# Performance work log

Measured on AMD Instinct MI355X. Metric: run time of the kernel, lower is better.

The kernel has to match this reference:

```python
import jax, jax.numpy as jnp
import numpy as np

B, L, T = 256, 1024, 128


def setup_inputs() -> dict:
    key = jax.random.key(0)
    k1, k2, k3, k4 = jax.random.split(key, 4)
    inputs = jax.random.normal(k1, (B, L, T), dtype=jnp.float32)
    lengths = jax.random.randint(k2, (B,), 1, L + 1, dtype=jnp.int32)
    tags = jax.random.randint(k3, (B, L), 0, T, dtype=jnp.int32)
    # learned CRF transition matrix (random_normal_initializer default stddev=0.05)
    transition_params = jax.random.normal(k4, (T, T), dtype=jnp.float32) * 0.05
    return {"inputs": inputs, "lengths": lengths, "tags": tags,
            "transition_params": transition_params}


def _crf_decode(x, trans, lengths):
    """Viterbi decode. x: [B,L,T], trans: [T,T], lengths: [B] -> tags [B,L] int32."""
    Bx, Lx, Tx = x.shape

    def fwd_step(state, inp):
        x_t, t = inp  # x_t: [B,T]
        scores = state[:, :, None] + trans[None]          # [B, T_prev, T_cur]
        bp = jnp.argmax(scores, axis=1).astype(jnp.int32)  # [B,T]
        new_state = jnp.max(scores, axis=1) + x_t           # [B,T]
        m = (t < lengths)[:, None]
        state = jnp.where(m, new_state, state)
        bp = jnp.where(m, bp, 0)
        return state, bp

    init = x[:, 0]                                          # [B,T]
    xs = (jnp.swapaxes(x[:, 1:], 0, 1), jnp.arange(1, Lx))
    state, bps = jax.lax.scan(fwd_step, init, xs)           # bps: [L-1,B,T]
    bps = jnp.concatenate([jnp.zeros((1, Bx, Tx), jnp.int32), bps], axis=0)  # bp[0] unused
    last_tag = jnp.argmax(state, axis=-1).astype(jnp.int32)  # [B] tag at position length-1

    def bwd_step(carry, inp):
        bp_t, t = inp
        emit = jnp.where(t < lengths, carry, 0)             # tags beyond length -> 0
        prev = jnp.take_along_axis(bp_t, carry[:, None], axis=1)[:, 0]
        carry = jnp.where((t > 0) & (t < lengths), prev, carry)
        return carry, emit

    _, tags_rev = jax.lax.scan(bwd_step, last_tag, (bps[::-1], jnp.arange(Lx)[::-1]))
    return jnp.swapaxes(tags_rev[::-1], 0, 1)               # [B,L]


def reference(inputs, lengths, tags, transition_params):
    # Decoder.call: tfa.text.crf_decode(inputs, transition_params, lengths)[0]
    return _crf_decode(inputs, transition_params, lengths)
```

## Files before the change

kernel.cpp:

```cpp
#include <hip/hip_runtime.h>

#define BB 256
#define LL 1024
#define TT 128
#define NTH 512

__device__ __forceinline__ void lds_barrier() {
    asm volatile("s_waitcnt lgkmcnt(0)\n\ts_barrier" ::);
}

struct SmallSmem {
    float state[TT];
    float pv[NTH];
    int   pi[NTH];
    unsigned char tags[LL];
};

__global__ __launch_bounds__(NTH)
void viterbi_kernel(const float* __restrict__ x,
                    const int* __restrict__ lengths,
                    const float* __restrict__ trans,
                    int* __restrict__ out) {
    __shared__ SmallSmem sm;
    extern __shared__ unsigned char bp[];

    const int b   = blockIdx.x;
    const int tid = threadIdx.x;
    const int j   = tid & (TT - 1);
    const int q   = tid >> 7;

    int lenb = lengths[b];
    if (lenb < 1) lenb = 1;
    if (lenb > LL) lenb = LL;

    float tc[32];
    #pragma unroll
    for (int ii = 0; ii < 32; ++ii)
        tc[ii] = trans[(q * 32 + ii) * TT + j];

    const float* xb = x + (size_t)b * LL * TT;

    if (tid < TT) sm.state[tid] = xb[tid];

    float xv_cur = 0.0f, xv_next = 0.0f;
    if (tid < TT && lenb > 1) xv_cur = xb[TT + j];
    lds_barrier();

    for (int t = 1; t < lenb; ++t) {
        if (tid < TT) {
            int tn = (t + 1 < lenb) ? (t + 1) : (lenb - 1);
            xv_next = xb[tn * TT + j];
        }

        float best0 = -3.4e38f, best1 = -3.4e38f, best2 = -3.4e38f, best3 = -3.4e38f;
        int   bi0 = 0, bi1 = 1, bi2 = 2, bi3 = 3;
        const float4* st4 = reinterpret_cast<const float4*>(sm.state + q * 32);
        #pragma unroll
        for (int k = 0; k < 8; ++k) {
            float4 sv = st4[k];
            float s0 = sv.x + tc[4 * k + 0];
            float s1 = sv.y + tc[4 * k + 1];
            float s2 = sv.z + tc[4 * k + 2];
            float s3 = sv.w + tc[4 * k + 3];
            if (s0 > best0) { best0 = s0; bi0 = 4 * k + 0; }
            if (s1 > best1) { best1 = s1; bi1 = 4 * k + 1; }
            if (s2 > best2) { best2 = s2; bi2 = 4 * k + 2; }
            if (s3 > best3) { best3 = s3; bi3 = 4 * k + 3; }
        }
        float bb = best0; int bi = bi0;
        if (best1 > bb || (best1 == bb && bi1 < bi)) { bb = best1; bi = bi1; }
        if (best2 > bb || (best2 == bb && bi2 < bi)) { bb = best2; bi = bi2; }
        if (best3 > bb || (best3 == bb && bi3 < bi)) { bb = best3; bi = bi3; }
        sm.pv[tid] = bb;
        sm.pi[tid] = bi + q * 32;
        lds_barrier();

        if (tid < TT) {
            float bv = sm.pv[j];       int ix = sm.pi[j];
            float v1 = sm.pv[j + 128]; int i1 = sm.pi[j + 128];
            float v2 = sm.pv[j + 256]; int i2 = sm.pi[j + 256];
            float v3 = sm.pv[j + 384]; int i3 = sm.pi[j + 384];
            if (v1 > bv) { bv = v1; ix = i1; }
            if (v2 > bv) { bv = v2; ix = i2; }
            if (v3 > bv) { bv = v3; ix = i3; }
            sm.state[j] = bv + xv_cur;
            bp[t * TT + j] = (unsigned char)ix;
            xv_cur = xv_next;
        }
        lds_barrier();
    }

    if (tid == 0) {
        float bv = sm.state[0]; int ix = 0;
        for (int i = 1; i < TT; ++i) {
            float v = sm.state[i];
            if (v > bv) { bv = v; ix = i; }
        }
        int carry = ix;
        for (int t = lenb - 1; t >= 1; --t) {
            sm.tags[t] = (unsigned char)carry;
            carry = bp[t * TT + carry];
        }
        sm.tags[0] = (unsigned char)carry;
    }
    lds_barrier();

    int* outb = out + (size_t)b * LL;
    for (int t = tid; t < LL; t += NTH)
        outb[t] = (t < lenb) ? (int)sm.tags[t] : 0;
}

extern "C" void kernel_launch(void* const* d_in, const int* in_sizes, int n_in,
                              void* d_out, int out_size, void* d_ws, size_t ws_size,
                              hipStream_t stream) {
    const float* x       = (const float*)d_in[0];
    const int*   lengths = (const int*)d_in[1];
    const float* trans   = (const float*)d_in[3];
    int*         out     = (int*)d_out;

    const int dyn = LL * TT;
    hipFuncSetAttribute((const void*)&viterbi_kernel,
                        hipFuncAttributeMaxDynamicSharedMemorySize, dyn);
    viterbi_kernel<<<BB, NTH, dyn, stream>>>(x, lengths, trans, out);
}
```

Measured before the change: 934.7 us.

## Double block threads and reduce argmax partials across lanes with shuffles

Raises the block size from 512 to 1024 threads, so each thread scans 16 predecessor states instead of 32. The second-stage reduction of the 8 partial maxima now runs across all threads, with each group of 8 lanes combining partials through xor shuffles. This replaces the serial 4-way combine done by only 128 threads. The partial arrays are padded (stride 132) to avoid LDS bank conflicts. The cost is more threads per barrier and a shuffle tree on every sequential timestep.

```diff
diff --git a/kernel.cpp b/kernel.cpp
--- a/kernel.cpp
+++ b/kernel.cpp
@@ -3,7 +3,10 @@
 #define BB 256
 #define LL 1024
 #define TT 128
-#define NTH 512
+#define NTH 1024
+#define NG 8
+#define PG 16
+#define PVS 132
 
 __device__ __forceinline__ void lds_barrier() {
     asm volatile("s_waitcnt lgkmcnt(0)\n\ts_barrier" ::);
@@ -11,8 +14,8 @@
 
 struct SmallSmem {
     float state[TT];
-    float pv[NTH];
-    int   pi[NTH];
+    float pv[NG * PVS];
+    int   pi[NG * PVS];
     unsigned char tags[LL];
 };
 
@@ -27,66 +30,69 @@
     const int b   = blockIdx.x;
     const int tid = threadIdx.x;
     const int j   = tid & (TT - 1);
-    const int q   = tid >> 7;
+    const int g   = tid >> 7;
+    const int jm  = tid >> 3;
+    const int wm  = tid & 7;
 
     int lenb = lengths[b];
     if (lenb < 1) lenb = 1;
     if (lenb > LL) lenb = LL;
 
-    float tc[32];
+    float tc[PG];
     #pragma unroll
-    for (int ii = 0; ii < 32; ++ii)
-        tc[ii] = trans[(q * 32 + ii) * TT + j];
+    for (int ii = 0; ii < PG; ++ii)
+        tc[ii] = trans[(g * PG + ii) * TT + j];
 
     const float* xb = x + (size_t)b * LL * TT;
 
     if (tid < TT) sm.state[tid] = xb[tid];
 
     float xv_cur = 0.0f, xv_next = 0.0f;
-    if (tid < TT && lenb > 1) xv_cur = xb[TT + j];
+    if (lenb > 1) xv_cur = xb[TT + jm];
     lds_barrier();
 
     for (int t = 1; t < lenb; ++t) {
-        if (tid < TT) {
+        {
             int tn = (t + 1 < lenb) ? (t + 1) : (lenb - 1);
-            xv_next = xb[tn * TT + j];
+            xv_next = xb[tn * TT + jm];
         }
 
-        float best0 = -3.4e38f, best1 = -3.4e38f, best2 = -3.4e38f, best3 = -3.4e38f;
-        int   bi0 = 0, bi1 = 1, bi2 = 2, bi3 = 3;
-        const float4* st4 = reinterpret_cast<const float4*>(sm.state + q * 32);
+        float a0 = -3.4e38f, a1 = -3.4e38f, a2 = -3.4e38f, a3 = -3.4e38f;
+        int   i0 = 0, i1 = 1, i2 = 2, i3 = 3;
+        const float4* st4 = reinterpret_cast<const float4*>(sm.state + g * PG);
         #pragma unroll
-        for (int k = 0; k < 8; ++k) {
+        for (int k = 0; k < 4; ++k) {
             float4 sv = st4[k];
             float s0 = sv.x + tc[4 * k + 0];
             float s1 = sv.y + tc[4 * k + 1];
             float s2 = sv.z + tc[4 * k + 2];
             float s3 = sv.w + tc[4 * k + 3];
-            if (s0 > best0) { best0 = s0; bi0 = 4 * k + 0; }
-            if (s1 > best1) { best1 = s1; bi1 = 4 * k + 1; }
-            if (s2 > best2) { best2 = s2; bi2 = 4 * k + 2; }
-            if (s3 > best3) { best3 = s3; bi3 = 4 * k + 3; }
+            if (s0 > a0) { a0 = s0; i0 = 4 * k + 0; }
+            if (s1 > a1) { a1 = s1; i1 = 4 * k + 1; }
+            if (s2 > a2) { a2 = s2; i2 = 4 * k + 2; }
+            if (s3 > a3) { a3 = s3; i3 = 4 * k + 3; }
         }
-        float bb = best0; int bi = bi0;
-        if (best1 > bb || (best1 == bb && bi1 < bi)) { bb = best1; bi = bi1; }
-        if (best2 > bb || (best2 == bb && bi2 < bi)) { bb = best2; bi = bi2; }
-        if (best3 > bb || (best3 == bb && bi3 < bi)) { bb = best3; bi = bi3; }
-        sm.pv[tid] = bb;
-        sm.pi[tid] = bi + q * 32;
+        float av = a0; int ax = i0;
+        if (a1 > av || (a1 == av && i1 < ax)) { av = a1; ax = i1; }
+        if (a2 > av || (a2 == av && i2 < ax)) { av = a2; ax = i2; }
+        if (a3 > av || (a3 == av && i3 < ax)) { av = a3; ax = i3; }
+        sm.pv[g * PVS + j] = av;
+        sm.pi[g * PVS + j] = ax + g * PG;
         lds_barrier();
 
-        if (tid < TT) {
-            float bv = sm.pv[j];       int ix = sm.pi[j];
-            float v1 = sm.pv[j + 128]; int i1 = sm.pi[j + 128];
-            float v2 = sm.pv[j + 256]; int i2 = sm.pi[j + 256];
-            float v3 = sm.pv[j + 384]; int i3 = sm.pi[j + 384];
-            if (v1 > bv) { bv = v1; ix = i1; }
-            if (v2 > bv) { bv = v2; ix = i2; }
-            if (v3 > bv) { bv = v3; ix = i3; }
-            sm.state[j] = bv + xv_cur;
-            bp[t * TT + j] = (unsigned char)ix;
-            xv_cur = xv_next;
+        float mv = sm.pv[wm * PVS + jm];
+        int   mi = sm.pi[wm * PVS + jm];
+        #pragma unroll
+        for (int m = 1; m <= 4; m <<= 1) {
+            float ov = __shfl_xor(mv, m, 64);
+            int   oi = __shfl_xor(mi, m, 64);
+            if (ov > mv || (ov == mv && oi < mi)) { mv = ov; mi = oi; }
         }
+        if (wm == 0) {
+            sm.state[jm] = mv + xv_cur;
+            bp[t * TT + jm] = (unsigned char)mi;
+        }
+        xv_cur = xv_next;
         lds_barrier();
     }
 
```

Result: slower. 1.309 ms (+40.0%).
